# Optimization experiments

Measured on AMD Instinct MI355X. Metric: run time of the kernel, lower is better.

Reference implementation:

```python
import jax, jax.numpy as jnp
import numpy as np

EPS = 1e-6
N_HEADS = 16

def setup_inputs() -> dict:
    key = jax.random.key(0)
    ks = jax.random.split(key, 5)
    B, N, D = 64, 512, 1024
    x = jax.random.normal(ks[0], (B, N, D), dtype=jnp.float32)
    s = 0.02
    W_q = jax.random.normal(ks[1], (D, D), dtype=jnp.float32) * s
    W_k = jax.random.normal(ks[2], (D, D), dtype=jnp.float32) * s
    W_v = jax.random.normal(ks[3], (D, D), dtype=jnp.float32) * s
    W_o = jax.random.normal(ks[4], (D, D), dtype=jnp.float32) * s
    z = jnp.zeros((D,), dtype=jnp.float32)
    return {"x": x, "W_q": W_q, "b_q": z, "W_k": W_k, "b_k": z,
            "W_v": W_v, "b_v": z, "W_o": W_o, "b_o": z}

def _heads(t, B, N, H, Dk):
    # [B,N,H*Dk] -> [B,H,N,Dk]
    return t.reshape(B, N, H, Dk).transpose(0, 2, 1, 3)

def reference(x, W_q, b_q, W_k, b_k, W_v, b_v, W_o, b_o):
    B, N, Dm = x.shape
    H = N_HEADS
    Dk = Dm // H
    q = _heads(x @ W_q.T + b_q, B, N, H, Dk)
    k = _heads(x @ W_k.T + b_k, B, N, H, Dk)
    v = _heads(x @ W_v.T + b_v, B, N, H, Dk)
    # position decay LUT: exp(-n/N), applied to ReLU feature maps of q and k
    dec = jnp.exp(-jnp.arange(N, dtype=jnp.float32) / N)[None, None, :, None]
    qf = jax.nn.relu(q) * dec  # [B,H,N,Dk]
    kf = jax.nn.relu(k) * dec
    # global (non-causal) summaries: KV = sum_n k_n v_n^T, Ksum = sum_n k_n
    KV = jnp.einsum('bhnd,bhne->bhde', kf, v)      # [B,H,Dk,Dk]
    Ksum = kf.sum(axis=2)                           # [B,H,Dk]
    denom = jnp.einsum('bhnd,bhd->bhn', qf, Ksum) + EPS
    out = jnp.einsum('bhnd,bhde->bhne', qf, KV) / denom[..., None]
    out = out.transpose(0, 2, 1, 3).reshape(B, N, Dm)
    return out @ W_o.T + b_o
```

## Files before the change

### kernel.cpp

```cpp
#include <hip/hip_runtime.h>
#include <hip/hip_bf16.h>

typedef __attribute__((ext_vector_type(8))) __bf16 bf16x8;
typedef __attribute__((ext_vector_type(4))) __bf16 bf16x4;
typedef __attribute__((ext_vector_type(4))) float f32x4;

#define NBATCH 64
#define NSEQ   512
#define DMODEL 1024
#define NHEAD  16
#define DHEAD  64
#define MROWS  (NBATCH * NSEQ)

static __device__ __forceinline__ void gload_lds16(const void* gp, void* lp) {
  __builtin_amdgcn_global_load_lds(
      (__attribute__((address_space(1))) const void*)gp,
      (__attribute__((address_space(3))) void*)lp,
      16, 0, 0);
}

__global__ void cvt_all_kernel(const float* __restrict__ x, const float* __restrict__ Wq,
                               const float* __restrict__ Wk, const float* __restrict__ Wv,
                               const float* __restrict__ Wo,
                               __bf16* __restrict__ xb, __bf16* __restrict__ Wqkvb,
                               __bf16* __restrict__ Wob) {
  constexpr int NX = (MROWS * DMODEL) / 4;
  constexpr int NW = (DMODEL * DMODEL) / 4;
  int i = blockIdx.x * blockDim.x + threadIdx.x;
  const int stride = gridDim.x * blockDim.x;
  for (; i < NX + 4 * NW; i += stride) {
    const float* src; __bf16* dst; int idx;
    if (i < NX)            { src = x;  dst = xb;             idx = i; }
    else if (i < NX + NW)  { src = Wq; dst = Wqkvb;          idx = i - NX; }
    else if (i < NX + 2*NW){ src = Wk; dst = Wqkvb + 4*NW;   idx = i - NX - NW; }
    else if (i < NX + 3*NW){ src = Wv; dst = Wqkvb + 8*NW;   idx = i - NX - 2*NW; }
    else                   { src = Wo; dst = Wob;            idx = i - NX - 3*NW; }
    const float4 v = reinterpret_cast<const float4*>(src)[idx];
    bf16x4 o;
    o.x = (__bf16)v.x; o.y = (__bf16)v.y; o.z = (__bf16)v.z; o.w = (__bf16)v.w;
    reinterpret_cast<bf16x4*>(dst)[idx] = o;
  }
}

template <int MODE>
__global__ __launch_bounds__(512, 1)
void gemm256_kernel(const __bf16* __restrict__ A, const __bf16* __restrict__ Bw,
                    const float* __restrict__ bias0, const float* __restrict__ bias1,
                    const float* __restrict__ bias2,
                    __bf16* __restrict__ outq, __bf16* __restrict__ outkT,
                    __bf16* __restrict__ outvT, float* __restrict__ outf) {
  extern __shared__ char smem[];
  constexpr int K = 1024;
  constexpr int NT = K / 64;
  constexpr int NBN = (MODE == 0) ? 12 : 4;
  constexpr int NWG = 128 * NBN;
  constexpr int CPX = NWG / 8;

  const int raw = blockIdx.x;
  const int wgid = (raw & 7) * CPX + (raw >> 3);
  const int bm = wgid / NBN;
  const int bn = wgid - bm * NBN;
  const int m0 = bm * 256, j0 = bn * 256;

  const int tid = threadIdx.x;
  const int l = tid & 63;
  const int w = tid >> 6;
  const int wm = w >> 2, wn = w & 3;
  const int lrow = l & 15, g16 = l >> 4;

  f32x4 acc[8][4] = {};

  auto stage = [&](int part, int tileIdx) {
    const int mat = part >> 1, kh = part & 1;
    const int buf = tileIdx & 1;
    char* region = smem + (((buf << 2) | (mat << 1) | kh) << 14);
    const __bf16* src = mat ? Bw : A;
    const int rowbase = mat ? j0 : m0;
    const int kk = tileIdx * 64 + kh * 32;
#pragma unroll
    for (int i = 0; i < 2; i++) {
      const int Q = i * 8192 + tid * 16;
      const int Ls = Q ^ (((Q >> 7) & 3) << 4);
      gload_lds16(src + (size_t)(rowbase + (Ls >> 6)) * K + kk + ((Ls & 63) >> 1),
                  region + Q);
    }
  };

  auto ldfrag = [&](int mat, int kh, int buf, int row) -> bf16x8 {
    const int L = row * 64 + g16 * 16;
    const int phys = L ^ (((row >> 1) & 3) << 4);
    return *reinterpret_cast<const bf16x8*>(
        smem + (((buf << 2) | (mat << 1) | kh) << 14) + phys);
  };

  stage(0, 0); stage(2, 0); stage(3, 0); stage(1, 0);
  asm volatile("s_waitcnt vmcnt(0)" ::: "memory");
  __builtin_amdgcn_s_barrier();

  const int arow = wm * 128 + lrow;
  const int brow = wn * 64 + lrow;

  for (int T = 0; T < NT; T++) {
    const int buf = T & 1;
    const bool pre = (T + 1 < NT);
    if (pre) { stage(0, T + 1); stage(2, T + 1); }
    bf16x8 a0[4], b0[4], a1[4];
#pragma unroll
    for (int mi = 0; mi < 4; mi++) a0[mi] = ldfrag(0, 0, buf, arow + mi * 16);
#pragma unroll
    for (int ni = 0; ni < 4; ni++) b0[ni] = ldfrag(1, 0, buf, brow + ni * 16);
#pragma unroll
    for (int mi = 0; mi < 4; mi++) a1[mi] = ldfrag(0, 0, buf, arow + 64 + mi * 16);
    if (pre) { stage(3, T + 1); stage(1, T + 1); }
    __builtin_amdgcn_s_setprio(1);
#pragma unroll
    for (int mi = 0; mi < 4; mi++)
#pragma unroll
      for (int ni = 0; ni < 4; ni++)
        acc[mi][ni] = __builtin_amdgcn_mfma_f32_16x16x32_bf16(a0[mi], b0[ni], acc[mi][ni], 0, 0, 0);
    __builtin_amdgcn_s_setprio(0);
    bf16x8 a0n[4];
#pragma unroll
    for (int mi = 0; mi < 4; mi++) a0n[mi] = ldfrag(0, 1, buf, arow + mi * 16);
    __builtin_amdgcn_s_setprio(1);
#pragma unroll
    for (int mi = 0; mi < 4; mi++)
#pragma unroll
      for (int ni = 0; ni < 4; ni++)
        acc[4 + mi][ni] = __builtin_amdgcn_mfma_f32_16x16x32_bf16(a1[mi], b0[ni], acc[4 + mi][ni], 0, 0, 0);
    __builtin_amdgcn_s_setprio(0);
    bf16x8 b1[4], a1n[4];
#pragma unroll
    for (int ni = 0; ni < 4; ni++) b1[ni] = ldfrag(1, 1, buf, brow + ni * 16);
#pragma unroll
    for (int mi = 0; mi < 4; mi++) a1n[mi] = ldfrag(0, 1, buf, arow + 64 + mi * 16);
    __builtin_amdgcn_s_setprio(1);
#pragma unroll
    for (int mi = 0; mi < 4; mi++)
#pragma unroll
      for (int ni = 0; ni < 4; ni++)
        acc[mi][ni] = __builtin_amdgcn_mfma_f32_16x16x32_bf16(a0n[mi], b1[ni], acc[mi][ni], 0, 0, 0);
#pragma unroll
    for (int mi = 0; mi < 4; mi++)
#pragma unroll
      for (int ni = 0; ni < 4; ni++)
        acc[4 + mi][ni] = __builtin_amdgcn_mfma_f32_16x16x32_bf16(a1n[mi], b1[ni], acc[4 + mi][ni], 0, 0, 0);
    __builtin_amdgcn_s_setprio(0);
    if (pre) {
      asm volatile("s_waitcnt vmcnt(0)" ::: "memory");
      __builtin_amdgcn_s_barrier();
    }
  }

  if constexpr (MODE == 0) {
    const int sel = j0 >> 10;
    const int jb = j0 & 1023;
    const float* bias = (sel == 0) ? bias0 : ((sel == 1) ? bias1 : bias2);
    float bj[4];
#pragma unroll
    for (int ni = 0; ni < 4; ni++) bj[ni] = bias[jb + wn * 64 + ni * 16 + lrow];
    if (sel == 0) {
#pragma unroll
      for (int mi = 0; mi < 8; mi++) {
        const int mbase = m0 + wm * 128 + mi * 16 + g16 * 4;
#pragma unroll
        for (int r = 0; r < 4; r++) {
          const int m = mbase + r;
          const float dec = __expf(-(float)(m & (NSEQ - 1)) * (1.0f / NSEQ));
#pragma unroll
          for (int ni = 0; ni < 4; ni++) {
            const int j = jb + wn * 64 + ni * 16 + lrow;
            const float val = fmaxf(acc[mi][ni][r] + bj[ni], 0.f) * dec;
            outq[(size_t)m * DMODEL + j] = (__bf16)val;
          }
        }
      }
    } else {
#pragma unroll
      for (int mi = 0; mi < 8; mi++) {
        const int mbase = m0 + wm * 128 + mi * 16 + g16 * 4;
        const int bidx = mbase >> 9;
        const int n0 = mbase & (NSEQ - 1);
        float dec4[4];
        if (sel == 1) {
#pragma unroll
          for (int r = 0; r < 4; r++)
            dec4[r] = __expf(-(float)(n0 + r) * (1.0f / NSEQ));
        }
        __bf16* dst = (sel == 1) ? outkT : outvT;
#pragma unroll
        for (int ni = 0; ni < 4; ni++) {
          const int j = jb + wn * 64 + ni * 16 + lrow;
          bf16x4 pk;
#pragma unroll
          for (int r = 0; r < 4; r++) {
            float val = acc[mi][ni][r] + bj[ni];
            if (sel == 1) val = fmaxf(val, 0.f) * dec4[r];
            pk[r] = (__bf16)val;
          }
          *reinterpret_cast<bf16x4*>(
              &dst[((size_t)((bidx * NHEAD + (j >> 6)) * DHEAD + (j & 63))) * NSEQ + n0]) = pk;
        }
      }
    }
  } else {
#pragma unroll
    for (int mi = 0; mi < 8; mi++) {
      const int mbase = m0 + wm * 128 + mi * 16 + g16 * 4;
#pragma unroll
      for (int ni = 0; ni < 4; ni++) {
        const int j = j0 + wn * 64 + ni * 16 + lrow;
        const float bo = bias0[j];
#pragma unroll
        for (int r = 0; r < 4; r++)
          outf[(size_t)(mbase + r) * DMODEL + j] = acc[mi][ni][r] + bo;
      }
    }
  }
}

__global__ void attn_kernel(const __bf16* __restrict__ qf, const __bf16* __restrict__ kfT,
                            const __bf16* __restrict__ vT, __bf16* __restrict__ attn) {
  const int bh = blockIdx.x;
  const int b = bh >> 4, h = bh & 15;
  const __bf16* kT = kfT + (size_t)bh * DHEAD * NSEQ;
  const __bf16* vTp = vT + (size_t)bh * DHEAD * NSEQ;
  const __bf16* qp = qf + (size_t)b * NSEQ * DMODEL + h * DHEAD;
  __bf16* op = attn + (size_t)b * NSEQ * DMODEL + h * DHEAD;

  const int tid = threadIdx.x;
  const int l = tid & 63;
  const int w = tid >> 6;
  const int lrow = l & 15, lk = (l >> 4) * 8;

  __shared__ __bf16 KVT[64][88];
  __shared__ float Ksum[64];
  __shared__ float ksum_part[4][64];
  __shared__ float denom[512];

  {
    f32x4 kv[4] = {};
    const int arow = w * 16 + lrow;
    for (int kk = 0; kk < NSEQ; kk += 32) {
      bf16x8 a = *reinterpret_cast<const bf16x8*>(&kT[(size_t)arow * NSEQ + kk + lk]);
#pragma unroll
      for (int ni = 0; ni < 4; ni++) {
        bf16x8 bv = *reinterpret_cast<const bf16x8*>(&vTp[(size_t)(ni * 16 + lrow) * NSEQ + kk + lk]);
        kv[ni] = __builtin_amdgcn_mfma_f32_16x16x32_bf16(a, bv, kv[ni], 0, 0, 0);
      }
    }
    const int d0 = w * 16 + ((l >> 4) << 2);
#pragma unroll
    for (int ni = 0; ni < 4; ni++) {
      const int e = ni * 16 + lrow;
      bf16x4 pk;
#pragma unroll
      for (int r = 0; r < 4; r++) pk[r] = (__bf16)kv[ni][r];
      *reinterpret_cast<bf16x4*>(&KVT[e][d0]) = pk;
    }
  }

  {
    const int d = tid & 63, part = tid >> 6;
    float s = 0.f;
    for (int n = part * 128; n < part * 128 + 128; n += 8) {
      bf16x8 kv8 = *reinterpret_cast<const bf16x8*>(&kT[(size_t)d * NSEQ + n]);
#pragma unroll
      for (int j = 0; j < 8; j++) s += (float)kv8[j];
    }
    ksum_part[part][d] = s;
  }
  __syncthreads();
  if (tid < 64)
    Ksum[tid] = ksum_part[0][tid] + ksum_part[1][tid] + ksum_part[2][tid] + ksum_part[3][tid];
  __syncthreads();

  for (int n = tid; n < NSEQ; n += 256) {
    float s = 0.f;
#pragma unroll
    for (int d = 0; d < DHEAD; d += 8) {
      bf16x8 q8 = *reinterpret_cast<const bf16x8*>(&qp[(size_t)n * DMODEL + d]);
#pragma unroll
      for (int j = 0; j < 8; j++) s += (float)q8[j] * Ksum[d + j];
    }
    denom[n] = s + 1e-6f;
  }
  __syncthreads();

  for (int t = 0; t < 8; t++) {
    const int nrow = t * 64 + w * 16 + lrow;
    bf16x8 a0 = *reinterpret_cast<const bf16x8*>(&qp[(size_t)nrow * DMODEL + lk]);
    bf16x8 a1 = *reinterpret_cast<const bf16x8*>(&qp[(size_t)nrow * DMODEL + 32 + lk]);
    f32x4 o[4] = {};
#pragma unroll
    for (int ni = 0; ni < 4; ni++) {
      bf16x8 b0 = *reinterpret_cast<const bf16x8*>(&KVT[ni * 16 + lrow][lk]);
      bf16x8 b1 = *reinterpret_cast<const bf16x8*>(&KVT[ni * 16 + lrow][32 + lk]);
      o[ni] = __builtin_amdgcn_mfma_f32_16x16x32_bf16(a0, b0, o[ni], 0, 0, 0);
      o[ni] = __builtin_amdgcn_mfma_f32_16x16x32_bf16(a1, b1, o[ni], 0, 0, 0);
    }
    const int n0 = t * 64 + w * 16 + ((l >> 4) << 2);
#pragma unroll
    for (int ni = 0; ni < 4; ni++) {
      const int e = ni * 16 + lrow;
#pragma unroll
      for (int r = 0; r < 4; r++)
        op[(size_t)(n0 + r) * DMODEL + e] = (__bf16)(o[ni][r] / denom[n0 + r]);
    }
  }
}

extern "C" void kernel_launch(void* const* d_in, const int* in_sizes, int n_in,
                              void* d_out, int out_size, void* d_ws, size_t ws_size,
                              hipStream_t stream) {
  (void)in_sizes; (void)n_in; (void)out_size; (void)ws_size;
  const float* x  = (const float*)d_in[0];
  const float* Wq = (const float*)d_in[1];
  const float* bq = (const float*)d_in[2];
  const float* Wk = (const float*)d_in[3];
  const float* bk = (const float*)d_in[4];
  const float* Wv = (const float*)d_in[5];
  const float* bv = (const float*)d_in[6];
  const float* Wo = (const float*)d_in[7];
  const float* bo = (const float*)d_in[8];
  float* out = (float*)d_out;

  char* ws = (char*)d_ws;
  __bf16* xb    = (__bf16*)(ws);
  __bf16* qf    = (__bf16*)(ws + 67108864);
  __bf16* kfT   = (__bf16*)(ws + 134217728);
  __bf16* vT    = (__bf16*)(ws + 201326592);
  __bf16* Wqkvb = (__bf16*)(ws + 268435456);
  __bf16* Wob   = (__bf16*)(ws + 274726912);
  __bf16* attnb = xb;

  cvt_all_kernel<<<4096, 256, 0, stream>>>(x, Wq, Wk, Wv, Wo, xb, Wqkvb, Wob);

  gemm256_kernel<0><<<1536, 512, 131072, stream>>>(xb, Wqkvb, bq, bk, bv,
                                                   qf, kfT, vT, nullptr);
  attn_kernel<<<NBATCH * NHEAD, 256, 0, stream>>>(qf, kfT, vT, attnb);
  gemm256_kernel<1><<<512, 512, 131072, stream>>>(attnb, Wob, bo, nullptr, nullptr,
                                                  nullptr, nullptr, nullptr, out);
}
```

Baseline: 437.7 us.

## Restructure GEMM main loop into 4-phase ping-pong with partial vmcnt waits

The GEMM K-loop is split into four phases. Each phase loads one set of LDS fragments, issues one quarter of the next tile's global-to-LDS loads, then runs a 16-MFMA block, with barriers between phases. Prefetch runs further ahead: some quarters for tile T+2 are issued early, and the end-of-tile wait uses vmcnt(4) instead of draining all loads. The goal is better overlap of global loads and LDS reads with MFMA work, at the cost of more barriers per tile and tighter buffer-reuse ordering.

```diff
diff --git a/kernel.cpp b/kernel.cpp
--- a/kernel.cpp
+++ b/kernel.cpp
@@ -70,8 +70,7 @@
 
   f32x4 acc[8][4] = {};
 
-  auto stage = [&](int part, int tileIdx) {
-    const int mat = part >> 1, kh = part & 1;
+  auto stage2 = [&](int mat, int kh, int tileIdx) {
     const int buf = tileIdx & 1;
     char* region = smem + (((buf << 2) | (mat << 1) | kh) << 14);
     const __bf16* src = mat ? Bw : A;
@@ -93,25 +92,24 @@
         smem + (((buf << 2) | (mat << 1) | kh) << 14) + phys);
   };
 
-  stage(0, 0); stage(2, 0); stage(3, 0); stage(1, 0);
-  asm volatile("s_waitcnt vmcnt(0)" ::: "memory");
+  stage2(0, 0, 0); stage2(1, 0, 0); stage2(0, 1, 0); stage2(1, 1, 0);
+  stage2(0, 0, 1); stage2(1, 0, 1);
+  asm volatile("s_waitcnt vmcnt(4)" ::: "memory");
   __builtin_amdgcn_s_barrier();
 
   const int arow = wm * 128 + lrow;
   const int brow = wn * 64 + lrow;
 
-  for (int T = 0; T < NT; T++) {
-    const int buf = T & 1;
-    const bool pre = (T + 1 < NT);
-    if (pre) { stage(0, T + 1); stage(2, T + 1); }
-    bf16x8 a0[4], b0[4], a1[4];
+  auto tile = [&](int T, int buf) {
+    bf16x8 a0[4], b0[4];
 #pragma unroll
     for (int mi = 0; mi < 4; mi++) a0[mi] = ldfrag(0, 0, buf, arow + mi * 16);
 #pragma unroll
     for (int ni = 0; ni < 4; ni++) b0[ni] = ldfrag(1, 0, buf, brow + ni * 16);
-#pragma unroll
-    for (int mi = 0; mi < 4; mi++) a1[mi] = ldfrag(0, 0, buf, arow + 64 + mi * 16);
-    if (pre) { stage(3, T + 1); stage(1, T + 1); }
+    if (T + 1 < NT) stage2(0, 1, T + 1);
+    asm volatile("" ::: "memory");
+    __builtin_amdgcn_s_barrier();
+    asm volatile("s_waitcnt lgkmcnt(0)" ::: "memory");
     __builtin_amdgcn_s_setprio(1);
 #pragma unroll
     for (int mi = 0; mi < 4; mi++)
@@ -119,9 +117,15 @@
       for (int ni = 0; ni < 4; ni++)
         acc[mi][ni] = __builtin_amdgcn_mfma_f32_16x16x32_bf16(a0[mi], b0[ni], acc[mi][ni], 0, 0, 0);
     __builtin_amdgcn_s_setprio(0);
-    bf16x8 a0n[4];
-#pragma unroll
-    for (int mi = 0; mi < 4; mi++) a0n[mi] = ldfrag(0, 1, buf, arow + mi * 16);
+    asm volatile("" ::: "memory");
+    __builtin_amdgcn_s_barrier();
+    bf16x8 a1[4];
+#pragma unroll
+    for (int mi = 0; mi < 4; mi++) a1[mi] = ldfrag(0, 0, buf, arow + 64 + mi * 16);
+    if (T + 1 < NT) stage2(1, 1, T + 1);
+    asm volatile("" ::: "memory");
+    __builtin_amdgcn_s_barrier();
+    asm volatile("s_waitcnt lgkmcnt(0)" ::: "memory");
     __builtin_amdgcn_s_setprio(1);
 #pragma unroll
     for (int mi = 0; mi < 4; mi++)
@@ -129,28 +133,48 @@
       for (int ni = 0; ni < 4; ni++)
         acc[4 + mi][ni] = __builtin_amdgcn_mfma_f32_16x16x32_bf16(a1[mi], b0[ni], acc[4 + mi][ni], 0, 0, 0);
     __builtin_amdgcn_s_setprio(0);
-    bf16x8 b1[4], a1n[4];
+    asm volatile("" ::: "memory");
+    __builtin_amdgcn_s_barrier();
+    bf16x8 a2[4], b1[4];
+#pragma unroll
+    for (int mi = 0; mi < 4; mi++) a2[mi] = ldfrag(0, 1, buf, arow + mi * 16);
 #pragma unroll
     for (int ni = 0; ni < 4; ni++) b1[ni] = ldfrag(1, 1, buf, brow + ni * 16);
-#pragma unroll
-    for (int mi = 0; mi < 4; mi++) a1n[mi] = ldfrag(0, 1, buf, arow + 64 + mi * 16);
+    if (T + 2 < NT) stage2(0, 0, T + 2);
+    asm volatile("" ::: "memory");
+    __builtin_amdgcn_s_barrier();
+    asm volatile("s_waitcnt lgkmcnt(0)" ::: "memory");
     __builtin_amdgcn_s_setprio(1);
 #pragma unroll
     for (int mi = 0; mi < 4; mi++)
 #pragma unroll
       for (int ni = 0; ni < 4; ni++)
-        acc[mi][ni] = __builtin_amdgcn_mfma_f32_16x16x32_bf16(a0n[mi], b1[ni], acc[mi][ni], 0, 0, 0);
+        acc[mi][ni] = __builtin_amdgcn_mfma_f32_16x16x32_bf16(a2[mi], b1[ni], acc[mi][ni], 0, 0, 0);
+    __builtin_amdgcn_s_setprio(0);
+    asm volatile("" ::: "memory");
+    __builtin_amdgcn_s_barrier();
+    bf16x8 a3[4];
+#pragma unroll
+    for (int mi = 0; mi < 4; mi++) a3[mi] = ldfrag(0, 1, buf, arow + 64 + mi * 16);
+    if (T + 2 < NT) stage2(1, 0, T + 2);
+    asm volatile("" ::: "memory");
+    __builtin_amdgcn_s_barrier();
+    asm volatile("s_waitcnt lgkmcnt(0)" ::: "memory");
+    __builtin_amdgcn_s_setprio(1);
 #pragma unroll
     for (int mi = 0; mi < 4; mi++)
 #pragma unroll
       for (int ni = 0; ni < 4; ni++)
-        acc[4 + mi][ni] = __builtin_amdgcn_mfma_f32_16x16x32_bf16(a1n[mi], b1[ni], acc[4 + mi][ni], 0, 0, 0);
+        acc[4 + mi][ni] = __builtin_amdgcn_mfma_f32_16x16x32_bf16(a3[mi], b1[ni], acc[4 + mi][ni], 0, 0, 0);
     __builtin_amdgcn_s_setprio(0);
-    if (pre) {
-      asm volatile("s_waitcnt vmcnt(0)" ::: "memory");
+    if (T < NT - 1) {
+      if (T < NT - 2)  asm volatile("s_waitcnt vmcnt(4)" ::: "memory");
+      else             asm volatile("s_waitcnt vmcnt(0)" ::: "memory");
       __builtin_amdgcn_s_barrier();
     }
-  }
+  };
+
+  for (int Tb = 0; Tb < NT; Tb += 2) { tile(Tb, 0); tile(Tb + 1, 1); }
 
   if constexpr (MODE == 0) {
     const int sel = j0 >> 10;
```

After: 436.6 us. Within noise of the previous version (-0.2%).
